# Performance work log

Hardware: AMD Instinct MI355X
Metric: run time of the kernel (lower is better)

## Reference

```python
import jax, jax.numpy as jnp
import numpy as np

UNK_ID = 0
EPS = 1e-20


def setup_inputs() -> dict:
    key = jax.random.key(0)
    k1, k2, k3, k4, k5 = jax.random.split(key, 5)
    bs, ls, vocab, emb = 8, 256, 32000, 100
    return {
        "logits": jax.random.normal(k1, (bs, ls, vocab), dtype=jnp.float32),
        "gumbel_u": jax.random.uniform(k2, (bs, ls, vocab), dtype=jnp.float32),
        "inp_word": jax.random.randint(k3, (bs, ls), 0, vocab, dtype=jnp.int64),
        "obf_mask": jax.random.randint(k4, (bs, ls), 0, 2, dtype=jnp.int32),
        "parser_emb_weight": jax.random.normal(k5, (vocab, emb), dtype=jnp.float32),
    }


def reference(logits, gumbel_u, inp_word, obf_mask, parser_emb_weight):
    # dec ends in LogSoftmax -> gen_logits are log-probs
    lp = jax.nn.log_softmax(logits, axis=-1)                       # [b,s,V]
    mask = obf_mask.astype(bool)                                   # [b,s]
    vocab = lp.shape[-1]

    # ent_loss = mean over masked rows of lp * exp(lp)
    ent_all = jnp.sum(lp * jnp.exp(lp), axis=-1)                   # [b,s]
    n_masked = jnp.sum(mask).astype(lp.dtype)
    ent_loss = jnp.sum(jnp.where(mask, ent_all, 0.0)) / (n_masked * vocab)

    # gumbel_softmax(targeted_logits, temperature=1.0) -- eval mode
    g = -jnp.log(-jnp.log(gumbel_u + EPS) + EPS)
    relaxed = jax.nn.softmax(lp + g, axis=-1)                      # [b,s,V]
    sampled_idx = jnp.argmax(relaxed, axis=-1)                     # [b,s]
    sampled_emb = jnp.einsum('bsv,vd->bsd', relaxed, parser_emb_weight)

    # masked_scatter_ chains collapse to per-position selects:
    #   masked & safe   -> sampled_idx / sampled_emb
    #   masked & unsafe -> UNK_ID / W[UNK_ID]
    #   unmasked        -> inp_word / W[inp_word]
    safe = sampled_idx != inp_word                                 # [b,s]
    obf_word = jnp.where(mask, jnp.where(safe, sampled_idx, UNK_ID), inp_word)
    base_emb = parser_emb_weight[inp_word]                         # [b,s,d]
    unk_emb = parser_emb_weight[UNK_ID]                            # [d]
    obf_word_emb = jnp.where(
        mask[..., None],
        jnp.where(safe[..., None], sampled_emb, unk_emb),
        base_emb,
    )
    return obf_word, obf_word_emb, ent_loss
```

## Files before the change

### kernel.cpp

```cpp
#include <hip/hip_runtime.h>

#define P_TOT   2048
#define V       32000
#define D       100
#define DPAD    128
#define TS      16
#define VSPLIT  10
#define KB      3200
#define VC      128
#define NCHUNK  25
#define ASTRIDE 136
#define BSTRIDE 136
#define BTILE_BYTES (DPAD * BSTRIDE * 2)

typedef __attribute__((ext_vector_type(8))) short short8;
typedef __attribute__((ext_vector_type(4))) float floatx4;

static __device__ __forceinline__ unsigned short f2bf(float x) {
    unsigned u = __float_as_uint(x);
    u += 0x7FFFu + ((u >> 16) & 1u);
    return (unsigned short)(u >> 16);
}

static __device__ __forceinline__ void gload_lds16(const void* g, void* l) {
    __builtin_amdgcn_global_load_lds(
        (const __attribute__((address_space(1))) unsigned int*)g,
        (__attribute__((address_space(3))) unsigned int*)l, 16, 0, 0);
}

__global__ __launch_bounds__(256)
void k_prep(const float* __restrict__ W, unsigned short* __restrict__ Wtp) {
    __shared__ float tile[VC * 101];
    const int ch = blockIdx.x, vs = blockIdx.y;
    const int vbase = vs * KB + ch * VC;
    const int tid = threadIdx.x;
    const float* src = W + (size_t)vbase * D;
    for (int idx = tid; idx < VC * D; idx += 256) {
        int vl = idx / D, d = idx - vl * D;
        tile[vl * 101 + d] = src[idx];
    }
    __syncthreads();
    unsigned short* dst = Wtp + (size_t)(vs * NCHUNK + ch) * (DPAD * BSTRIDE);
    for (int idx = tid; idx < DPAD * BSTRIDE; idx += 256) {
        int d = idx / BSTRIDE, e = idx - d * BSTRIDE;
        float v = (d < D && e < VC) ? tile[e * 101 + d] : 0.0f;
        dst[idx] = f2bf(v);
    }
}

__global__ __launch_bounds__(256, 4)
void k_main(const float* __restrict__ logits, const float* __restrict__ gum,
            const unsigned short* __restrict__ Wtp,
            float* __restrict__ Epart, float* __restrict__ stats) {
    __shared__ __align__(16) unsigned short Abuf[TS * ASTRIDE];
    __shared__ __align__(16) unsigned short Bbuf[DPAD * BSTRIDE];
    __shared__ __align__(16) float alphaS[TS];
    __shared__ float m2run[TS], s2run[TS], amaxv[TS];
    __shared__ int amaxi[TS];

    const int tid   = threadIdx.x;
    const int r     = tid >> 4;
    const int q     = tid & 15;
    const int lane  = tid & 63;
    const int w     = tid >> 6;
    const int stile = blockIdx.x;
    const int vs    = blockIdx.y;

    const int grow = stile * TS + r;
    const size_t rowbase = (size_t)grow * V + (size_t)vs * KB;

    if (tid < TS) {
        m2run[tid] = -1e30f; s2run[tid] = 0.0f;
        amaxv[tid] = -1e30f; amaxi[tid] = 0;
    }

    float m1 = -1e30f, sA = 0.0f, sB = 0.0f;
    floatx4 acc[2];
    acc[0] = (floatx4){0.f, 0.f, 0.f, 0.f};
    acc[1] = (floatx4){0.f, 0.f, 0.f, 0.f};

    const float* lbase = logits + rowbase + q * 8;
    const float* ubase = gum    + rowbase + q * 8;

    float4 cl0 = *(const float4*)(lbase);
    float4 cl1 = *(const float4*)(lbase + 4);
    float4 cu0 = *(const float4*)(ubase);
    float4 cu1 = *(const float4*)(ubase + 4);

    const char* wsrc = (const char*)Wtp + (size_t)vs * NCHUNK * BTILE_BYTES
                     + (size_t)lane * 16;

    for (int ch = 0; ch < NCHUNK; ++ch) {
        const int cbase = ch * VC;

        __syncthreads();

        {
            const char* src = wsrc + (size_t)ch * BTILE_BYTES;
            char* dstb = (char*)Bbuf;
            #pragma unroll
            for (int it = 0; it < 8; ++it) {
                int k = it * 4 + w;
                gload_lds16(src + k * 1024, dstb + k * 1024);
            }
            if (w < 2) {
                int k = 32 + w;
                gload_lds16(src + k * 1024, dstb + k * 1024);
            }
        }

        float4 nl0, nl1, nu0, nu1;
        if (ch + 1 < NCHUNK) {
            const float* lp = lbase + cbase + VC;
            const float* up = ubase + cbase + VC;
            nl0 = *(const float4*)(lp);
            nl1 = *(const float4*)(lp + 4);
            nu0 = *(const float4*)(up);
            nu1 = *(const float4*)(up + 4);
        }

        float lg[8], zz[8];
        {
            float la[8] = {cl0.x, cl0.y, cl0.z, cl0.w, cl1.x, cl1.y, cl1.z, cl1.w};
            float ua[8] = {cu0.x, cu0.y, cu0.z, cu0.w, cu1.x, cu1.y, cu1.z, cu1.w};
            #pragma unroll
            for (int j = 0; j < 8; ++j) {
                lg[j] = la[j];
                float g = -logf(-logf(ua[j] + 1e-20f) + 1e-20f);
                zz[j] = la[j] + g;
            }
        }

        {
            float cm = lg[0];
            #pragma unroll
            for (int j = 1; j < 8; ++j) cm = fmaxf(cm, lg[j]);
            float m1n = fmaxf(m1, cm);
            float sc = __expf(m1 - m1n);
            sB = (sB + sA * (m1 - m1n)) * sc;
            sA = sA * sc;
            m1 = m1n;
            #pragma unroll
            for (int j = 0; j < 8; ++j) {
                float t = lg[j] - m1;
                float e = __expf(t);
                sA += e; sB += t * e;
            }
        }

        float cmv = -1e30f; int cmi = 0;
        #pragma unroll
        for (int j = 0; j < 8; ++j) {
            int gidx = vs * KB + cbase + q * 8 + j;
            if (zz[j] > cmv) { cmv = zz[j]; cmi = gidx; }
        }
        #pragma unroll
        for (int m = 1; m < 16; m <<= 1) {
            float ov = __shfl_xor(cmv, m, 64);
            int   oi = __shfl_xor(cmi, m, 64);
            if (ov > cmv || (ov == cmv && oi < cmi)) { cmv = ov; cmi = oi; }
        }

        float m2old = m2run[r];
        float m2new = fmaxf(m2old, cmv);
        float csum = 0.0f;
        unsigned short pb[8];
        #pragma unroll
        for (int j = 0; j < 8; ++j) {
            float p = __expf(zz[j] - m2new);
            csum += p;
            pb[j] = f2bf(p);
        }
        *(ushort4*)(&Abuf[r * ASTRIDE + q * 8])     = make_ushort4(pb[0], pb[1], pb[2], pb[3]);
        *(ushort4*)(&Abuf[r * ASTRIDE + q * 8 + 4]) = make_ushort4(pb[4], pb[5], pb[6], pb[7]);
        #pragma unroll
        for (int m = 1; m < 16; m <<= 1) csum += __shfl_xor(csum, m, 64);
        if (q == 0) {
            float al = __expf(m2old - m2new);
            alphaS[r] = al;
            s2run[r] = s2run[r] * al + csum;
            m2run[r] = m2new;
            if (cmv > amaxv[r]) { amaxv[r] = cmv; amaxi[r] = cmi; }
        }

        __syncthreads();

        floatx4 al4 = *(const floatx4*)(&alphaS[(lane >> 4) << 2]);
        #pragma unroll
        for (int nt = 0; nt < 2; ++nt) {
            acc[nt][0] *= al4[0]; acc[nt][1] *= al4[1];
            acc[nt][2] *= al4[2]; acc[nt][3] *= al4[3];
        }
        const int ka0 = (lane >> 4) << 3;
        const unsigned short* arow = &Abuf[(lane & 15) * ASTRIDE + ka0];
        #pragma unroll
        for (int ks = 0; ks < 4; ++ks) {
            short8 a = *(const short8*)(arow + ks * 32);
            #pragma unroll
            for (int nt = 0; nt < 2; ++nt) {
                const unsigned short* brow =
                    &Bbuf[(w * 32 + nt * 16 + (lane & 15)) * BSTRIDE + ka0 + ks * 32];
                short8 b = *(const short8*)brow;
                acc[nt] = __builtin_amdgcn_mfma_f32_16x16x32_bf16(a, b, acc[nt], 0, 0, 0);
            }
        }

        if (ch + 1 < NCHUNK) { cl0 = nl0; cl1 = nl1; cu0 = nu0; cu1 = nu1; }
    }

    #pragma unroll
    for (int m = 1; m < 16; m <<= 1) {
        float om = __shfl_xor(m1, m, 64);
        float oA = __shfl_xor(sA, m, 64);
        float oB = __shfl_xor(sB, m, 64);
        float mn = fmaxf(m1, om);
        float ea = __expf(m1 - mn), eb = __expf(om - mn);
        sB = (sB + sA * (m1 - mn)) * ea + (oB + oA * (om - mn)) * eb;
        sA = sA * ea + oA * eb;
        m1 = mn;
    }
    if (q == 0) {
        float* st = stats + ((size_t)grow * VSPLIT + vs) * 8;
        st[0] = m1; st[1] = sA; st[2] = sB;
        st[3] = m2run[r]; st[4] = s2run[r];
        st[5] = amaxv[r]; st[6] = __int_as_float(amaxi[r]); st[7] = 0.0f;
    }
    #pragma unroll
    for (int nt = 0; nt < 2; ++nt) {
        int n = w * 32 + nt * 16 + (lane & 15);
        if (n < D) {
            #pragma unroll
            for (int i = 0; i < 4; ++i) {
                int row = ((lane >> 4) << 2) + i;
                int pos = stile * TS + row;
                Epart[((size_t)pos * VSPLIT + vs) * D + n] = acc[nt][i];
            }
        }
    }
}

__global__ __launch_bounds__(128)
void k_combine(const float* __restrict__ stats, const float* __restrict__ Epart,
               const float* __restrict__ W, const int* __restrict__ inp,
               const int* __restrict__ msk, float* __restrict__ out,
               float* __restrict__ entbuf) {
    const int pos = blockIdx.x;
    const int t = threadIdx.x;
    const float* st = stats + (size_t)pos * VSPLIT * 8;

    float m1 = -1e30f, sA = 0.0f, sB = 0.0f, m2g = -1e30f;
    float bestv = -1e30f; int besti = 0;
    #pragma unroll
    for (int p = 0; p < VSPLIT; ++p) {
        const float* s = st + p * 8;
        float om = s[0], oA = s[1], oB = s[2];
        float mn = fmaxf(m1, om);
        float ea = __expf(m1 - mn), eb = __expf(om - mn);
        sB = (sB + sA * (m1 - mn)) * ea + (oB + oA * (om - mn)) * eb;
        sA = sA * ea + oA * eb;
        m1 = mn;
        m2g = fmaxf(m2g, s[3]);
        float av = s[5];
        if (av > bestv) { bestv = av; besti = __float_as_int(s[6]); }
    }
    float beta[VSPLIT];
    float s2g = 0.0f;
    #pragma unroll
    for (int p = 0; p < VSPLIT; ++p) {
        beta[p] = __expf(st[p*8 + 3] - m2g);
        s2g += st[p*8 + 4] * beta[p];
    }

    const int iw = inp[pos];
    const bool mk = msk[pos] != 0;
    const bool safe = besti != iw;

    if (t == 0) {
        int obf = mk ? (safe ? besti : 0) : iw;
        out[pos] = (float)obf;
        float ent = sB / sA - logf(sA);
        entbuf[pos] = mk ? ent : 0.0f;
    }
    if (t < D) {
        float e = 0.0f;
        const float* ep = Epart + (size_t)pos * VSPLIT * D + t;
        #pragma unroll
        for (int p = 0; p < VSPLIT; ++p) e += ep[(size_t)p * D] * beta[p];
        e /= s2g;
        float val;
        if (mk) val = safe ? e : W[t];
        else    val = W[(size_t)iw * D + t];
        out[P_TOT + (size_t)pos * D + t] = val;
    }
}

__global__ __launch_bounds__(256)
void k_final(const float* __restrict__ entbuf, const int* __restrict__ msk,
             float* __restrict__ out) {
    __shared__ float se[4], sm[4];
    const int t = threadIdx.x;
    float e = 0.0f, m = 0.0f;
    for (int i = t; i < P_TOT; i += 256) {
        e += entbuf[i];
        m += (float)msk[i];
    }
    #pragma unroll
    for (int k = 32; k >= 1; k >>= 1) {
        e += __shfl_down(e, k, 64);
        m += __shfl_down(m, k, 64);
    }
    if ((t & 63) == 0) { se[t >> 6] = e; sm[t >> 6] = m; }
    __syncthreads();
    if (t == 0) {
        float te = se[0] + se[1] + se[2] + se[3];
        float tm = sm[0] + sm[1] + sm[2] + sm[3];
        out[P_TOT + (size_t)P_TOT * D] = te / (tm * (float)V);
    }
}

extern "C" void kernel_launch(void* const* d_in, const int* in_sizes, int n_in,
                              void* d_out, int out_size, void* d_ws, size_t ws_size,
                              hipStream_t stream) {
    const float* logits = (const float*)d_in[0];
    const float* gum    = (const float*)d_in[1];
    const int*   inp    = (const int*)d_in[2];
    const int*   msk    = (const int*)d_in[3];
    const float* W      = (const float*)d_in[4];
    float* out = (float*)d_out;

    char* ws = (char*)d_ws;
    unsigned short* Wtp = (unsigned short*)ws;
    float* Epart  = (float*)(ws + 8704000);
    float* stats  = (float*)(ws + 16896000);
    float* entbuf = (float*)(ws + 17551360);

    k_prep<<<dim3(NCHUNK, VSPLIT), 256, 0, stream>>>(W, Wtp);
    dim3 g1(P_TOT / TS, VSPLIT);
    k_main<<<g1, 256, 0, stream>>>(logits, gum, Wtp, Epart, stats);
    k_combine<<<P_TOT, 128, 0, stream>>>(stats, Epart, W, inp, msk, out, entbuf);
    k_final<<<1, 256, 0, stream>>>(entbuf, msk, out);
}
```

Before: 578.4 us.

## Halve vocab chunk, raise occupancy, remap blocks, use fast log and packed bf16

Shrinks the per-iteration vocab chunk from 128 to 64 with a tighter LDS stride so blocks use less shared memory and registers, and raises launch bounds to 8 waves per SIMD. Blocks move to a 1D grid with a strided remap that spreads vocab splits across XCDs. The Gumbel noise now uses fast __logf for the softmax path, with precise logf recomputed only for the argmax candidate and a fallback when the top two are within a small margin. Probabilities are packed with v_cvt_pk_bf16. The fast log adds small numerical error to the softmax weights, and twice as many chunk iterations means twice as many barriers.

```diff
diff --git a/kernel.cpp b/kernel.cpp
--- a/kernel.cpp
+++ b/kernel.cpp
@@ -7,13 +7,14 @@
 #define TS      16
 #define VSPLIT  10
 #define KB      3200
-#define VC      128
-#define NCHUNK  25
-#define ASTRIDE 136
-#define BSTRIDE 136
-#define BTILE_BYTES (DPAD * BSTRIDE * 2)
+#define VC      64
+#define NCHUNK  50
+#define STRIDE  68
+#define BTILE   (DPAD * STRIDE)
+#define NSTILE  (P_TOT / TS)
 
 typedef __attribute__((ext_vector_type(8))) short short8;
+typedef __attribute__((ext_vector_type(4))) short short4v;
 typedef __attribute__((ext_vector_type(4))) float floatx4;
 
 static __device__ __forceinline__ unsigned short f2bf(float x) {
@@ -22,38 +23,50 @@
     return (unsigned short)(u >> 16);
 }
 
+static __device__ __forceinline__ unsigned cvt_pk_bf16(float lo, float hi) {
+    unsigned r;
+    asm("v_cvt_pk_bf16_f32 %0, %1, %2" : "=v"(r) : "v"(lo), "v"(hi));
+    return r;
+}
+
 static __device__ __forceinline__ void gload_lds16(const void* g, void* l) {
     __builtin_amdgcn_global_load_lds(
         (const __attribute__((address_space(1))) unsigned int*)g,
         (__attribute__((address_space(3))) unsigned int*)l, 16, 0, 0);
 }
 
+static __device__ __forceinline__ short8 lds_frag(const unsigned short* p) {
+    short4v lo = *(const short4v*)p;
+    short4v hi = *(const short4v*)(p + 4);
+    short8 v = {lo[0], lo[1], lo[2], lo[3], hi[0], hi[1], hi[2], hi[3]};
+    return v;
+}
+
 __global__ __launch_bounds__(256)
 void k_prep(const float* __restrict__ W, unsigned short* __restrict__ Wtp) {
     __shared__ float tile[VC * 101];
     const int ch = blockIdx.x, vs = blockIdx.y;
-    const int vbase = vs * KB + ch * VC;
     const int tid = threadIdx.x;
-    const float* src = W + (size_t)vbase * D;
+    const float* src = W + (size_t)(vs * KB + ch * VC) * D;
     for (int idx = tid; idx < VC * D; idx += 256) {
         int vl = idx / D, d = idx - vl * D;
         tile[vl * 101 + d] = src[idx];
     }
     __syncthreads();
-    unsigned short* dst = Wtp + (size_t)(vs * NCHUNK + ch) * (DPAD * BSTRIDE);
-    for (int idx = tid; idx < DPAD * BSTRIDE; idx += 256) {
-        int d = idx / BSTRIDE, e = idx - d * BSTRIDE;
+    unsigned short* dst = Wtp + (size_t)(vs * NCHUNK + ch) * BTILE;
+    for (int idx = tid; idx < BTILE; idx += 256) {
+        int d = idx / STRIDE, e = idx - d * STRIDE;
         float v = (d < D && e < VC) ? tile[e * 101 + d] : 0.0f;
         dst[idx] = f2bf(v);
     }
 }
 
-__global__ __launch_bounds__(256, 4)
+__global__ __launch_bounds__(256, 8)
 void k_main(const float* __restrict__ logits, const float* __restrict__ gum,
             const unsigned short* __restrict__ Wtp,
             float* __restrict__ Epart, float* __restrict__ stats) {
-    __shared__ __align__(16) unsigned short Abuf[TS * ASTRIDE];
-    __shared__ __align__(16) unsigned short Bbuf[DPAD * BSTRIDE];
+    __shared__ __align__(16) unsigned short Abuf[TS * STRIDE];
+    __shared__ __align__(16) unsigned short Bbuf[DPAD * STRIDE];
     __shared__ __align__(16) float alphaS[TS];
     __shared__ float m2run[TS], s2run[TS], amaxv[TS];
     __shared__ int amaxi[TS];
@@ -63,8 +76,11 @@
     const int q     = tid & 15;
     const int lane  = tid & 63;
     const int w     = tid >> 6;
-    const int stile = blockIdx.x;
-    const int vs    = blockIdx.y;
+
+    const int bid   = blockIdx.x;
+    const int gidxb = (bid & 7) * (NSTILE * VSPLIT / 8) + (bid >> 3);
+    const int vs    = gidxb / NSTILE;
+    const int stile = gidxb - vs * NSTILE;
 
     const int grow = stile * TS + r;
     const size_t rowbase = (size_t)grow * V + (size_t)vs * KB;
@@ -79,15 +95,13 @@
     acc[0] = (floatx4){0.f, 0.f, 0.f, 0.f};
     acc[1] = (floatx4){0.f, 0.f, 0.f, 0.f};
 
-    const float* lbase = logits + rowbase + q * 8;
-    const float* ubase = gum    + rowbase + q * 8;
-
-    float4 cl0 = *(const float4*)(lbase);
-    float4 cl1 = *(const float4*)(lbase + 4);
-    float4 cu0 = *(const float4*)(ubase);
-    float4 cu1 = *(const float4*)(ubase + 4);
-
-    const char* wsrc = (const char*)Wtp + (size_t)vs * NCHUNK * BTILE_BYTES
+    const float* lbase = logits + rowbase + q * 4;
+    const float* ubase = gum    + rowbase + q * 4;
+
+    float4 cl = *(const float4*)(lbase);
+    float4 cu = *(const float4*)(ubase);
+
+    const char* wsrc = (const char*)Wtp + (size_t)vs * NCHUNK * (BTILE * 2)
                      + (size_t)lane * 16;
 
     for (int ch = 0; ch < NCHUNK; ++ch) {
@@ -96,64 +110,75 @@
         __syncthreads();
 
         {
-            const char* src = wsrc + (size_t)ch * BTILE_BYTES;
+            const char* src = wsrc + (size_t)ch * (BTILE * 2);
             char* dstb = (char*)Bbuf;
             #pragma unroll
-            for (int it = 0; it < 8; ++it) {
+            for (int it = 0; it < 4; ++it) {
                 int k = it * 4 + w;
                 gload_lds16(src + k * 1024, dstb + k * 1024);
             }
-            if (w < 2) {
-                int k = 32 + w;
-                gload_lds16(src + k * 1024, dstb + k * 1024);
-            }
-        }
-
-        float4 nl0, nl1, nu0, nu1;
+            if (w == 0) gload_lds16(src + 16 * 1024, dstb + 16 * 1024);
+        }
+
+        float4 nl, nu;
         if (ch + 1 < NCHUNK) {
-            const float* lp = lbase + cbase + VC;
-            const float* up = ubase + cbase + VC;
-            nl0 = *(const float4*)(lp);
-            nl1 = *(const float4*)(lp + 4);
-            nu0 = *(const float4*)(up);
-            nu1 = *(const float4*)(up + 4);
-        }
-
-        float lg[8], zz[8];
+            nl = *(const float4*)(lbase + cbase + VC);
+            nu = *(const float4*)(ubase + cbase + VC);
+        }
+
+        float lg[4] = {cl.x, cl.y, cl.z, cl.w};
+        float ua[4] = {cu.x, cu.y, cu.z, cu.w};
+        float zz[4];
+        #pragma unroll
+        for (int j = 0; j < 4; ++j) {
+            float g = -__logf(-__logf(ua[j] + 1e-20f) + 1e-20f);
+            zz[j] = lg[j] + g;
+        }
+
         {
-            float la[8] = {cl0.x, cl0.y, cl0.z, cl0.w, cl1.x, cl1.y, cl1.z, cl1.w};
-            float ua[8] = {cu0.x, cu0.y, cu0.z, cu0.w, cu1.x, cu1.y, cu1.z, cu1.w};
-            #pragma unroll
-            for (int j = 0; j < 8; ++j) {
-                lg[j] = la[j];
-                float g = -logf(-logf(ua[j] + 1e-20f) + 1e-20f);
-                zz[j] = la[j] + g;
-            }
-        }
-
-        {
-            float cm = lg[0];
-            #pragma unroll
-            for (int j = 1; j < 8; ++j) cm = fmaxf(cm, lg[j]);
+            float cm = fmaxf(fmaxf(lg[0], lg[1]), fmaxf(lg[2], lg[3]));
             float m1n = fmaxf(m1, cm);
             float sc = __expf(m1 - m1n);
             sB = (sB + sA * (m1 - m1n)) * sc;
             sA = sA * sc;
             m1 = m1n;
             #pragma unroll
-            for (int j = 0; j < 8; ++j) {
+            for (int j = 0; j < 4; ++j) {
                 float t = lg[j] - m1;
                 float e = __expf(t);
                 sA += e; sB += t * e;
             }
         }
 
-        float cmv = -1e30f; int cmi = 0;
-        #pragma unroll
-        for (int j = 0; j < 8; ++j) {
-            int gidx = vs * KB + cbase + q * 8 + j;
-            if (zz[j] > cmv) { cmv = zz[j]; cmi = gidx; }
-        }
+        float b1 = zz[0], b2 = -1e30f;
+        int bj = 0;
+        #pragma unroll
+        for (int j = 1; j < 4; ++j) {
+            bool gt = zz[j] > b1;
+            b2 = gt ? b1 : fmaxf(b2, zz[j]);
+            b1 = gt ? zz[j] : b1;
+            bj = gt ? j : bj;
+        }
+        float cmv; int cmi;
+        if (__builtin_expect(b2 > b1 - 1e-4f, 0)) {
+            cmv = -1e30f; cmi = 0;
+            #pragma unroll
+            for (int j = 0; j < 4; ++j) {
+                float zp = lg[j] - logf(-logf(ua[j] + 1e-20f) + 1e-20f);
+                if (zp > cmv) { cmv = zp; cmi = j; }
+            }
+        } else {
+            float bu = ua[0], bl = lg[0];
+            #pragma unroll
+            for (int j = 1; j < 4; ++j) {
+                bu = (bj == j) ? ua[j] : bu;
+                bl = (bj == j) ? lg[j] : bl;
+            }
+            cmv = bl - logf(-logf(bu + 1e-20f) + 1e-20f);
+            cmi = bj;
+        }
+        cmi += vs * KB + cbase + q * 4;
+
         #pragma unroll
         for (int m = 1; m < 16; m <<= 1) {
             float ov = __shfl_xor(cmv, m, 64);
@@ -163,16 +188,15 @@
 
         float m2old = m2run[r];
         float m2new = fmaxf(m2old, cmv);
-        float csum = 0.0f;
-        unsigned short pb[8];
-        #pragma unroll
-        for (int j = 0; j < 8; ++j) {
-            float p = __expf(zz[j] - m2new);
-            csum += p;
-            pb[j] = f2bf(p);
-        }
-        *(ushort4*)(&Abuf[r * ASTRIDE + q * 8])     = make_ushort4(pb[0], pb[1], pb[2], pb[3]);
-        *(ushort4*)(&Abuf[r * ASTRIDE + q * 8 + 4]) = make_ushort4(pb[4], pb[5], pb[6], pb[7]);
+        float p0 = __expf(zz[0] - m2new), p1 = __expf(zz[1] - m2new);
+        float p2 = __expf(zz[2] - m2new), p3 = __expf(zz[3] - m2new);
+        float csum = (p0 + p1) + (p2 + p3);
+        {
+            uint2 pk;
+            pk.x = cvt_pk_bf16(p0, p1);
+            pk.y = cvt_pk_bf16(p2, p3);
+            *(uint2*)(&Abuf[r * STRIDE + q * 4]) = pk;
+        }
         #pragma unroll
         for (int m = 1; m < 16; m <<= 1) csum += __shfl_xor(csum, m, 64);
         if (q == 0) {
@@ -192,20 +216,19 @@
             acc[nt][2] *= al4[2]; acc[nt][3] *= al4[3];
         }
         const int ka0 = (lane >> 4) << 3;
-        const unsigned short* arow = &Abuf[(lane & 15) * ASTRIDE + ka0];
-        #pragma unroll
-        for (int ks = 0; ks < 4; ++ks) {
-            short8 a = *(const short8*)(arow + ks * 32);
+        const unsigned short* arow = &Abuf[(lane & 15) * STRIDE + ka0];
+        #pragma unroll
+        for (int ks = 0; ks < 2; ++ks) {
+            short8 a = lds_frag(arow + ks * 32);
             #pragma unroll
             for (int nt = 0; nt < 2; ++nt) {
-                const unsigned short* brow =
-                    &Bbuf[(w * 32 + nt * 16 + (lane & 15)) * BSTRIDE + ka0 + ks * 32];
-                short8 b = *(const short8*)brow;
+                short8 b = lds_frag(
+                    &Bbuf[(w * 32 + nt * 16 + (lane & 15)) * STRIDE + ka0 + ks * 32]);
                 acc[nt] = __builtin_amdgcn_mfma_f32_16x16x32_bf16(a, b, acc[nt], 0, 0, 0);
             }
         }
 
-        if (ch + 1 < NCHUNK) { cl0 = nl0; cl1 = nl1; cu0 = nu0; cu1 = nu1; }
+        if (ch + 1 < NCHUNK) { cl = nl; cu = nu; }
     }
 
     #pragma unroll
@@ -335,8 +358,7 @@
     float* entbuf = (float*)(ws + 17551360);
 
     k_prep<<<dim3(NCHUNK, VSPLIT), 256, 0, stream>>>(W, Wtp);
-    dim3 g1(P_TOT / TS, VSPLIT);
-    k_main<<<g1, 256, 0, stream>>>(logits, gum, Wtp, Epart, stats);
+    k_main<<<NSTILE * VSPLIT, 256, 0, stream>>>(logits, gum, Wtp, Epart, stats);
     k_combine<<<P_TOT, 128, 0, stream>>>(stats, Epart, W, inp, msk, out, entbuf);
     k_final<<<1, 256, 0, stream>>>(entbuf, msk, out);
 }
```

Result: no change. 568.3 us (-1.7%).
